# Kernel optimization log

Measured on AMD Instinct MI355X. Metric: run time of the kernel, lower is better.

Reference implementation:

```python
import jax, jax.numpy as jnp
import numpy as np

N = 50000      # nodes
E = 400000     # edges (avg degree 8)
G = 256        # graphs in batch
H = 256        # hidden_dim
DEPTH = 6
A, C, X, EF = 16, 8, 3, 16  # a_t, c_t, x_t, e_t feature dims (node_feats=27)


def setup_inputs() -> dict:
    key = jax.random.key(0)
    ks = jax.random.split(key, 16)
    s = lambda i, shape, sc=1.0: jax.random.normal(ks[i], shape, jnp.float32) * sc
    return {
        "a_t": s(0, (N, A)),
        "c_t": s(1, (N, C)),
        "x_t": s(2, (N, X)),
        "e_t": s(3, (E, EF)),
        "src": jax.random.randint(ks[4], (E,), 0, N),
        "dst": jax.random.randint(ks[5], (E,), 0, N),
        "graph_id": jnp.sort(jax.random.randint(ks[6], (N,), 0, G)),
        "W_in": s(7, (A + C + X, H), 0.1), "b_in": jnp.zeros((H,), jnp.float32),
        "W_e": s(8, (EF, H), 0.1), "b_e": jnp.zeros((H,), jnp.float32),
        "Wc1": s(9, (DEPTH, H, H), 0.05), "bc1": jnp.zeros((DEPTH, H), jnp.float32),
        "g1": jnp.ones((DEPTH, H), jnp.float32), "be1": jnp.zeros((DEPTH, H), jnp.float32),
        "Wc2": s(10, (DEPTH, H, H), 0.05), "bc2": jnp.zeros((DEPTH, H), jnp.float32),
        "g2": jnp.ones((DEPTH, H), jnp.float32), "be2": jnp.zeros((DEPTH, H), jnp.float32),
        "W_head": s(11, (H, 1), 0.1), "b_head": jnp.zeros((1,), jnp.float32),
    }


def _ln(x, g, b):
    mu = jnp.mean(x, -1, keepdims=True)
    v = jnp.mean((x - mu) ** 2, -1, keepdims=True)
    return (x - mu) * jax.lax.rsqrt(v + 1e-5) * g + b


def reference(a_t, c_t, x_t, e_t, src, dst, graph_id,
              W_in, b_in, W_e, b_e,
              Wc1, bc1, g1, be1, Wc2, bc2, g2, be2,
              W_head, b_head):
    n = a_t.shape[0]
    ones_e = jnp.ones((src.shape[0],), jnp.float32)
    deg_out = jax.ops.segment_sum(ones_e, src, num_segments=n)
    deg_in = jax.ops.segment_sum(ones_e, dst, num_segments=n)
    # DGL GraphConv norm='both': 0 for isolated nodes (pow(0,-0.5)=inf -> 0)
    norm_o = jnp.where(deg_out > 0, jax.lax.rsqrt(jnp.maximum(deg_out, 1.0)), 0.0)
    norm_i = jnp.where(deg_in > 0, jax.lax.rsqrt(jnp.maximum(deg_in, 1.0)), 0.0)

    def gconv(x, W, b):
        h = (x * norm_o[:, None]) @ W            # [N,H] transform + src norm
        m = jax.ops.segment_sum(h[src], dst, num_segments=n)  # SpMM gather/scatter
        return m * norm_i[:, None] + b

    h = gconv(jnp.concatenate([a_t, c_t, x_t], -1), W_in, b_in)
    e = e_t @ W_e + b_e                          # edge_linear
    # copy_e + mean over in-edges
    e_mean = jax.ops.segment_sum(e, dst, num_segments=n) / jnp.maximum(deg_in, 1.0)[:, None]
    h = h + e_mean

    def body(hc, p):
        W1, b1, ga, ba, W2, b2, gb, bb = p
        t = jax.nn.silu(_ln(gconv(hc, W1, b1), ga, ba))
        t = jax.nn.silu(_ln(gconv(t, W2, b2), gb, bb))
        return t + hc, None  # skip is Identity (in_dim == out_dim)

    h, _ = jax.lax.scan(body, h, (Wc1, bc1, g1, be1, Wc2, bc2, g2, be2))

    cnt = jax.ops.segment_sum(jnp.ones((n,), jnp.float32), graph_id, num_segments=G)
    pooled = jax.ops.segment_sum(h, graph_id, num_segments=G) / jnp.maximum(cnt, 1.0)[:, None]
    # property='dipole' -> Softplus, tau=1.0
    return jax.nn.softplus((pooled @ W_head + b_head) / 1.0)
```

## Files before the change

### kernel.cpp

```cpp
#include <hip/hip_runtime.h>
#include <hip/hip_bf16.h>

#define N_NODES 50000
#define N_EDGES 400000
#define N_GRAPH 256
#define HID 256
#define DEPTH 6

typedef float f32x4 __attribute__((ext_vector_type(4)));
typedef int   i32x4 __attribute__((ext_vector_type(4)));

__device__ __forceinline__ float bf2f(unsigned short u) {
  unsigned v = ((unsigned)u) << 16;
  return __builtin_bit_cast(float, v);
}
__device__ __forceinline__ unsigned short f2bf(float f) {
  unsigned u = __builtin_bit_cast(unsigned, f);
  u += 0x7fffu + ((u >> 16) & 1u);
  return (unsigned short)(u >> 16);
}

__device__ __forceinline__ float block_sum256(float v, float* lds) {
#pragma unroll
  for (int off = 32; off > 0; off >>= 1) v += __shfl_down(v, off, 64);
  int w = threadIdx.x >> 6;
  if ((threadIdx.x & 63) == 0) lds[w] = v;
  __syncthreads();
  float r = lds[0] + lds[1] + lds[2] + lds[3];
  __syncthreads();
  return r;
}

__global__ __launch_bounds__(256) void k_deg(const int* __restrict__ src, const int* __restrict__ dst,
                                             int* deg_out, int* deg_in) {
  int e = blockIdx.x * 256 + threadIdx.x;
  if (e < N_EDGES) { atomicAdd(&deg_out[src[e]], 1); atomicAdd(&deg_in[dst[e]], 1); }
}

__global__ __launch_bounds__(256) void k_norm(const int* deg_out, const int* deg_in,
                                              float* norm_o, float* norm_i) {
  int i = blockIdx.x * 256 + threadIdx.x;
  if (i < N_NODES) {
    int dO = deg_out[i], dI = deg_in[i];
    norm_o[i] = dO > 0 ? rsqrtf((float)dO) : 0.f;
    norm_i[i] = dI > 0 ? rsqrtf((float)dI) : 0.f;
  }
}

__global__ __launch_bounds__(256) void k_scan1(const int* deg_in, int* partial) {
  int i = blockIdx.x * 256 + threadIdx.x;
  int v = (i < N_NODES) ? deg_in[i] : 0;
#pragma unroll
  for (int off = 32; off > 0; off >>= 1) v += __shfl_down(v, off, 64);
  __shared__ int l[4];
  if ((threadIdx.x & 63) == 0) l[threadIdx.x >> 6] = v;
  __syncthreads();
  if (threadIdx.x == 0) partial[blockIdx.x] = l[0] + l[1] + l[2] + l[3];
}

__global__ __launch_bounds__(256) void k_scan2(const int* partial, int* chunk_off, int* row_start, int nb) {
  __shared__ int ss[256];
  int t = threadIdx.x;
  int v = (t < nb) ? partial[t] : 0;
  ss[t] = v; __syncthreads();
#pragma unroll
  for (int off = 1; off < 256; off <<= 1) {
    int x = ss[t];
    int y = (t >= off) ? ss[t - off] : 0;
    __syncthreads();
    ss[t] = x + y;
    __syncthreads();
  }
  if (t < nb) chunk_off[t] = ss[t] - v;
  if (t == 0) row_start[N_NODES] = N_EDGES;
}

__global__ __launch_bounds__(256) void k_scan3(const int* deg_in, const int* chunk_off, int* row_start) {
  __shared__ int ss[256];
  int t = threadIdx.x;
  int i = blockIdx.x * 256 + t;
  int v = (i < N_NODES) ? deg_in[i] : 0;
  ss[t] = v; __syncthreads();
#pragma unroll
  for (int off = 1; off < 256; off <<= 1) {
    int x = ss[t];
    int y = (t >= off) ? ss[t - off] : 0;
    __syncthreads();
    ss[t] = x + y;
    __syncthreads();
  }
  if (i < N_NODES) row_start[i] = chunk_off[blockIdx.x] + ss[t] - v;
}

__global__ __launch_bounds__(256) void k_fill(const int* src, const int* dst, const int* row_start,
                                              int* cursor, int* csr_src) {
  int e = blockIdx.x * 256 + threadIdx.x;
  if (e < N_EDGES) {
    int d = dst[e];
    int p = atomicAdd(&cursor[d], 1);
    csr_src[row_start[d] + p] = src[e];
  }
}

__global__ __launch_bounds__(256) void k_esum(const float* __restrict__ e_t, const int* __restrict__ dst,
                                              float* esum) {
  int t = blockIdx.x * 256 + threadIdx.x;
  int e = t >> 4, ch = t & 15;
  if (e < N_EDGES) atomicAdd(&esum[(size_t)dst[e] * 16 + ch], e_t[(size_t)e * 16 + ch]);
}

__global__ __launch_bounds__(256) void k_wt(const float* __restrict__ Wc1, const float* __restrict__ Wc2,
                                            unsigned short* __restrict__ Wt) {
  __shared__ float tile[32][33];
  int li = blockIdx.z;
  const float* W = ((li & 1) ? Wc2 : Wc1) + (size_t)(li >> 1) * HID * HID;
  int k0 = blockIdx.x * 32, n0 = blockIdx.y * 32;
  int tx = threadIdx.x & 31, ty = threadIdx.x >> 5;
#pragma unroll
  for (int r = ty; r < 32; r += 8) tile[r][tx] = W[(size_t)(k0 + r) * HID + n0 + tx];
  __syncthreads();
  unsigned short* outp = Wt + (size_t)li * HID * HID;
#pragma unroll
  for (int r = ty; r < 32; r += 8) outp[(size_t)(n0 + r) * HID + k0 + tx] = f2bf(tile[tx][r]);
}

__global__ __launch_bounds__(256) void k_z(const float* __restrict__ a, const float* __restrict__ c,
                                           const float* __restrict__ x, const float* __restrict__ norm_o,
                                           float* __restrict__ z) {
  int t = blockIdx.x * 256 + threadIdx.x;
  int n = t >> 5, lane = t & 31;
  if (n >= N_NODES) return;
  float v = 0.f;
  if (lane < 16) v = a[(size_t)n * 16 + lane];
  else if (lane < 24) v = c[(size_t)n * 8 + (lane - 16)];
  else if (lane < 27) v = x[(size_t)n * 3 + (lane - 24)];
  z[(size_t)n * 32 + lane] = v * norm_o[n];
}

__global__ __launch_bounds__(256) void k_in(const float* __restrict__ z, const float* __restrict__ esum,
                                            const int* __restrict__ csr_src, const int* __restrict__ rs,
                                            const float* __restrict__ norm_o, const float* __restrict__ norm_i,
                                            const float* __restrict__ W_in, const float* __restrict__ b_in,
                                            const float* __restrict__ W_e, const float* __restrict__ b_e,
                                            unsigned short* __restrict__ hf, unsigned short* __restrict__ Af) {
  int w = threadIdx.x >> 6, lane = threadIdx.x & 63;
  int n = blockIdx.x * 4 + w;
  int half = lane >> 5, ch = lane & 31;
  __shared__ float zs[4][32];
  __shared__ float es[4][16];
  if (lane >= 32 && lane < 48) es[w][lane - 32] = esum[(size_t)n * 16 + (lane - 32)];
  int beg = rs[n], end = rs[n + 1];
  float acc = 0.f;
  const float* zb = z + ch;
  int p = beg + half;
  for (; p + 6 < end; p += 8) {
    int s0 = csr_src[p], s1 = csr_src[p + 2], s2 = csr_src[p + 4], s3 = csr_src[p + 6];
    float v0 = zb[(size_t)s0 * 32], v1 = zb[(size_t)s1 * 32];
    float v2 = zb[(size_t)s2 * 32], v3 = zb[(size_t)s3 * 32];
    acc += (v0 + v1) + (v2 + v3);
  }
  for (; p < end; p += 2) acc += zb[(size_t)csr_src[p] * 32];
  acc += __shfl_xor(acc, 32, 64);
  if (lane < 32) zs[w][ch] = acc;
  __syncthreads();
  float degf = (float)(end - beg);
  float invd = 1.f / fmaxf(degf, 1.f);
  float niv = norm_i[n], nov = norm_o[n];
#pragma unroll
  for (int i = 0; i < 4; ++i) {
    int cc = lane + 64 * i;
    float da = 0.f, de = 0.f;
#pragma unroll
    for (int k = 0; k < 27; ++k) da += zs[w][k] * W_in[k * HID + cc];
#pragma unroll
    for (int k = 0; k < 16; ++k) de += es[w][k] * W_e[k * HID + cc];
    float val = da * niv + b_in[cc] + (de + degf * b_e[cc]) * invd;
    hf[(size_t)n * HID + cc] = f2bf(val);
    Af[(size_t)n * HID + cc] = f2bf(val * nov);
  }
}

template <int RES>
__global__ __launch_bounds__(512) void k_layer(const unsigned short* __restrict__ Af,
                                               const int* __restrict__ csr_src, const int* __restrict__ rs,
                                               const unsigned short* __restrict__ Bt,
                                               const float* __restrict__ norm_i,
                                               const float* __restrict__ norm_o,
                                               const float* __restrict__ b, const float* __restrict__ g,
                                               const float* __restrict__ be,
                                               unsigned short* __restrict__ hf,
                                               unsigned short* __restrict__ AfN) {
  const int LDA = HID + 8;
  __shared__ unsigned short As[16 * LDA];
  __shared__ float red1[8][16], red2[8][16];
  int wave = threadIdx.x >> 6, lane = threadIdx.x & 63;
  int l15 = lane & 15, quad = lane >> 4;
  int n0 = blockIdx.x * 16;
  int off = lane * 4;
  int r0 = wave * 2;
  int beg = rs[n0 + r0], mid = rs[n0 + r0 + 1], end = rs[n0 + r0 + 2];
  float lo0 = 0.f, lo1 = 0.f, lo2 = 0.f, lo3 = 0.f;
  float hi0 = 0.f, hi1 = 0.f, hi2 = 0.f, hi3 = 0.f;
  int p = beg;
  for (; p + 8 <= end; p += 8) {
    int s[8];
#pragma unroll
    for (int q = 0; q < 8; ++q) s[q] = csr_src[p + q];
    ushort4 rr[8];
#pragma unroll
    for (int q = 0; q < 8; ++q) rr[q] = *(const ushort4*)(Af + (size_t)s[q] * HID + off);
#pragma unroll
    for (int q = 0; q < 8; ++q) {
      float v0 = bf2f(rr[q].x), v1 = bf2f(rr[q].y), v2 = bf2f(rr[q].z), v3 = bf2f(rr[q].w);
      if (p + q >= mid) { hi0 += v0; hi1 += v1; hi2 += v2; hi3 += v3; }
      else             { lo0 += v0; lo1 += v1; lo2 += v2; lo3 += v3; }
    }
  }
  for (; p < end; ++p) {
    ushort4 r = *(const ushort4*)(Af + (size_t)csr_src[p] * HID + off);
    float v0 = bf2f(r.x), v1 = bf2f(r.y), v2 = bf2f(r.z), v3 = bf2f(r.w);
    if (p >= mid) { hi0 += v0; hi1 += v1; hi2 += v2; hi3 += v3; }
    else          { lo0 += v0; lo1 += v1; lo2 += v2; lo3 += v3; }
  }
  ushort4 o;
  o.x = f2bf(lo0); o.y = f2bf(lo1); o.z = f2bf(lo2); o.w = f2bf(lo3);
  *(ushort4*)(&As[(size_t)r0 * LDA + off]) = o;
  o.x = f2bf(hi0); o.y = f2bf(hi1); o.z = f2bf(hi2); o.w = f2bf(hi3);
  *(ushort4*)(&As[(size_t)(r0 + 1) * LDA + off]) = o;
  __syncthreads();
  const unsigned short* asp = &As[(size_t)l15 * LDA + quad * 8];
  const unsigned short* bp = Bt + (size_t)(wave * 32 + l15) * HID + quad * 8;
  f32x4 acc[2] = {};
  asm volatile("s_nop 7\n\ts_nop 7" : "+v"(acc[0]), "+v"(acc[1]));
#pragma unroll
  for (int k0 = 0; k0 < HID; k0 += 32) {
    i32x4 af = *(const i32x4*)(asp + k0);
#pragma unroll
    for (int t = 0; t < 2; ++t) {
      i32x4 bt = *(const i32x4*)(bp + (size_t)t * 16 * HID + k0);
      asm volatile("v_mfma_f32_16x16x32_bf16 %0, %1, %2, %0" : "+v"(acc[t]) : "v"(af), "v"(bt));
    }
  }
  asm volatile("s_nop 7\n\ts_nop 7\n\ts_nop 7" : "+v"(acc[0]), "+v"(acc[1]));
  float ni[4];
#pragma unroll
  for (int j = 0; j < 4; ++j) ni[j] = norm_i[n0 + quad * 4 + j];
#pragma unroll
  for (int t = 0; t < 2; ++t) {
    int ct = wave * 32 + t * 16 + l15;
    float bv = b[ct];
#pragma unroll
    for (int j = 0; j < 4; ++j) acc[t][j] = acc[t][j] * ni[j] + bv;
  }
  float s1[4] = {0.f, 0.f, 0.f, 0.f}, s2[4] = {0.f, 0.f, 0.f, 0.f};
#pragma unroll
  for (int t = 0; t < 2; ++t)
#pragma unroll
    for (int j = 0; j < 4; ++j) { s1[j] += acc[t][j]; s2[j] += acc[t][j] * acc[t][j]; }
#pragma unroll
  for (int m = 1; m < 16; m <<= 1) {
#pragma unroll
    for (int j = 0; j < 4; ++j) {
      s1[j] += __shfl_xor(s1[j], m, 16);
      s2[j] += __shfl_xor(s2[j], m, 16);
    }
  }
  if (l15 == 0) {
#pragma unroll
    for (int j = 0; j < 4; ++j) {
      red1[wave][quad * 4 + j] = s1[j];
      red2[wave][quad * 4 + j] = s2[j];
    }
  }
  __syncthreads();
  float mu[4], inv[4];
#pragma unroll
  for (int j = 0; j < 4; ++j) {
    int r = quad * 4 + j;
    float t1 = 0.f, t2 = 0.f;
#pragma unroll
    for (int ww = 0; ww < 8; ++ww) { t1 += red1[ww][r]; t2 += red2[ww][r]; }
    mu[j] = t1 * (1.f / HID);
    float var = t2 * (1.f / HID) - mu[j] * mu[j];
    inv[j] = rsqrtf(var + 1e-5f);
  }
#pragma unroll
  for (int j = 0; j < 4; ++j) {
    int r = n0 + quad * 4 + j;
    float nov = norm_o[r];
    unsigned short* hrow = hf + (size_t)r * HID;
    unsigned short* an = AfN + (size_t)r * HID;
#pragma unroll
    for (int t = 0; t < 2; ++t) {
      int ct = wave * 32 + t * 16 + l15;
      float oo = (acc[t][j] - mu[j]) * inv[j] * g[ct] + be[ct];
      float sl = oo * (1.f / (1.f + __expf(-oo)));
      float outv = sl;
      if (RES) {
        outv = sl + bf2f(hrow[ct]);
        hrow[ct] = f2bf(outv);
      }
      an[ct] = f2bf(outv * nov);
    }
  }
}

__global__ __launch_bounds__(256) void k_poolhead(const unsigned short* __restrict__ hf,
                                                  const int* __restrict__ gid,
                                                  const float* __restrict__ Wh, const float* __restrict__ bh,
                                                  float* __restrict__ out) {
  int gg = blockIdx.x, ch = threadIdx.x;
  int lo = 0, hi = N_NODES;
  while (lo < hi) { int mid = (lo + hi) >> 1; if (gid[mid] < gg) lo = mid + 1; else hi = mid; }
  int beg = lo;
  hi = N_NODES;
  while (lo < hi) { int mid = (lo + hi) >> 1; if (gid[mid] < gg + 1) lo = mid + 1; else hi = mid; }
  int end = lo;
  float s = 0.f;
  int n = beg;
  for (; n + 4 <= end; n += 4) {
    s += bf2f(hf[(size_t)n * HID + ch]) + bf2f(hf[(size_t)(n + 1) * HID + ch]) +
         bf2f(hf[(size_t)(n + 2) * HID + ch]) + bf2f(hf[(size_t)(n + 3) * HID + ch]);
  }
  for (; n < end; ++n) s += bf2f(hf[(size_t)n * HID + ch]);
  float v = s * Wh[ch];
  __shared__ float l[4];
  float tot = block_sum256(v, l);
  if (ch == 0) {
    float c = fmaxf((float)(end - beg), 1.f);
    float xx = tot / c + bh[0];
    out[gg] = fmaxf(xx, 0.f) + log1pf(expf(-fabsf(xx)));
  }
}

extern "C" void kernel_launch(void* const* d_in, const int* in_sizes, int n_in,
                              void* d_out, int out_size, void* d_ws, size_t ws_size,
                              hipStream_t stream) {
  const float* a_t = (const float*)d_in[0];
  const float* c_t = (const float*)d_in[1];
  const float* x_t = (const float*)d_in[2];
  const float* e_t = (const float*)d_in[3];
  const int* src = (const int*)d_in[4];
  const int* dst = (const int*)d_in[5];
  const int* gid = (const int*)d_in[6];
  const float* W_in = (const float*)d_in[7];
  const float* b_in = (const float*)d_in[8];
  const float* W_e  = (const float*)d_in[9];
  const float* b_e  = (const float*)d_in[10];
  const float* Wc1  = (const float*)d_in[11];
  const float* bc1  = (const float*)d_in[12];
  const float* g1   = (const float*)d_in[13];
  const float* be1  = (const float*)d_in[14];
  const float* Wc2  = (const float*)d_in[15];
  const float* bc2  = (const float*)d_in[16];
  const float* g2   = (const float*)d_in[17];
  const float* be2  = (const float*)d_in[18];
  const float* W_head = (const float*)d_in[19];
  const float* b_head = (const float*)d_in[20];
  float* out = (float*)d_out;

  char* base = (char*)d_ws;
  size_t off = 0;
  auto carve = [&](size_t bytes) -> void* {
    void* p = base + off;
    off += (bytes + 255) & ~(size_t)255;
    return p;
  };
  int*   deg_out = (int*)carve((size_t)N_NODES * 4);
  int*   deg_in  = (int*)carve((size_t)N_NODES * 4);
  int*   cursor  = (int*)carve((size_t)N_NODES * 4);
  float* esum    = (float*)carve((size_t)N_NODES * 16 * 4);
  size_t zbytes = off;
  float* norm_o  = (float*)carve((size_t)N_NODES * 4);
  float* norm_i  = (float*)carve((size_t)N_NODES * 4);
  int*   row_start = (int*)carve((size_t)(N_NODES + 1) * 4);
  int*   partial   = (int*)carve(256 * 4);
  int*   chunk_off = (int*)carve(256 * 4);
  int*   csr_src   = (int*)carve((size_t)N_EDGES * 4);
  unsigned short* Wt = (unsigned short*)carve((size_t)2 * DEPTH * HID * HID * 2);
  float* zpack = (float*)carve((size_t)N_NODES * 32 * 4);
  unsigned short* hf = (unsigned short*)carve((size_t)N_NODES * HID * 2);
  unsigned short* Af0 = (unsigned short*)carve((size_t)N_NODES * HID * 2);
  unsigned short* Af1 = (unsigned short*)carve((size_t)N_NODES * HID * 2);
  (void)ws_size; (void)in_sizes; (void)n_in; (void)out_size;

  hipMemsetAsync(d_ws, 0, zbytes, stream);

  int ebl = (N_EDGES + 255) / 256;
  int nbl = (N_NODES + 255) / 256;
  k_deg<<<ebl, 256, 0, stream>>>(src, dst, deg_out, deg_in);
  k_norm<<<nbl, 256, 0, stream>>>(deg_out, deg_in, norm_o, norm_i);
  k_scan1<<<nbl, 256, 0, stream>>>(deg_in, partial);
  k_scan2<<<1, 256, 0, stream>>>(partial, chunk_off, row_start, nbl);
  k_scan3<<<nbl, 256, 0, stream>>>(deg_in, chunk_off, row_start);
  k_fill<<<ebl, 256, 0, stream>>>(src, dst, row_start, cursor, csr_src);
  k_esum<<<(N_EDGES * 16 + 255) / 256, 256, 0, stream>>>(e_t, dst, esum);
  k_wt<<<dim3(8, 8, 2 * DEPTH), 256, 0, stream>>>(Wc1, Wc2, Wt);
  k_z<<<(N_NODES * 32 + 255) / 256, 256, 0, stream>>>(a_t, c_t, x_t, norm_o, zpack);
  k_in<<<N_NODES / 4, 256, 0, stream>>>(zpack, esum, csr_src, row_start,
                                        norm_o, norm_i, W_in, b_in, W_e, b_e, hf, Af0);
  int gbl = N_NODES / 16;
  for (int d = 0; d < DEPTH; ++d) {
    k_layer<0><<<gbl, 512, 0, stream>>>(Af0, csr_src, row_start, Wt + (size_t)(2 * d) * HID * HID,
                                        norm_i, norm_o, bc1 + d * HID, g1 + d * HID, be1 + d * HID, hf, Af1);
    k_layer<1><<<gbl, 512, 0, stream>>>(Af1, csr_src, row_start, Wt + (size_t)(2 * d + 1) * HID * HID,
                                        norm_i, norm_o, bc2 + d * HID, g2 + d * HID, be2 + d * HID, hf, Af0);
  }
  k_poolhead<<<N_GRAPH, 256, 0, stream>>>(hf, gid, W_head, b_head, out);
}
```

Before: 1.443 ms.

## Use one node per wave in layer gather with 16-byte loads

The fused gather+GEMM layer kernel now handles 8 nodes per block instead of 16. Each wave gathers one node's neighbours, with its two half-waves splitting the edges and each lane loading 16 bytes (8 bf16). The partial sums are combined with a cross-half shuffle, and the unused MFMA rows are zero-padded. The input-layer gather is likewise vectorised to float4 per lane with 8 edges in flight. This aims to cut the divergent lo/hi accumulation and raise memory-level parallelism per wave, at the cost of doubling the block count and wasting half of each 16-row MFMA tile.

```diff
diff --git a/kernel.cpp b/kernel.cpp
--- a/kernel.cpp
+++ b/kernel.cpp
@@ -18,6 +18,12 @@
   unsigned u = __builtin_bit_cast(unsigned, f);
   u += 0x7fffu + ((u >> 16) & 1u);
   return (unsigned short)(u >> 16);
+}
+__device__ __forceinline__ float bflo(unsigned u) {
+  return __builtin_bit_cast(float, u << 16);
+}
+__device__ __forceinline__ float bfhi(unsigned u) {
+  return __builtin_bit_cast(float, u & 0xffff0000u);
 }
 
 __device__ __forceinline__ float block_sum256(float v, float* lds) {
@@ -145,23 +151,25 @@
                                             unsigned short* __restrict__ hf, unsigned short* __restrict__ Af) {
   int w = threadIdx.x >> 6, lane = threadIdx.x & 63;
   int n = blockIdx.x * 4 + w;
-  int half = lane >> 5, ch = lane & 31;
+  int g = lane >> 3, c4 = lane & 7;
   __shared__ float zs[4][32];
   __shared__ float es[4][16];
   if (lane >= 32 && lane < 48) es[w][lane - 32] = esum[(size_t)n * 16 + (lane - 32)];
   int beg = rs[n], end = rs[n + 1];
-  float acc = 0.f;
-  const float* zb = z + ch;
-  int p = beg + half;
-  for (; p + 6 < end; p += 8) {
-    int s0 = csr_src[p], s1 = csr_src[p + 2], s2 = csr_src[p + 4], s3 = csr_src[p + 6];
-    float v0 = zb[(size_t)s0 * 32], v1 = zb[(size_t)s1 * 32];
-    float v2 = zb[(size_t)s2 * 32], v3 = zb[(size_t)s3 * 32];
-    acc += (v0 + v1) + (v2 + v3);
-  }
-  for (; p < end; p += 2) acc += zb[(size_t)csr_src[p] * 32];
-  acc += __shfl_xor(acc, 32, 64);
-  if (lane < 32) zs[w][ch] = acc;
+  f32x4 acc = {0.f, 0.f, 0.f, 0.f};
+  for (int p = beg + g; p < end; p += 8) {
+    int s = csr_src[p];
+    acc += *(const f32x4*)(z + (size_t)s * 32 + c4 * 4);
+  }
+#pragma unroll
+  for (int m = 8; m < 64; m <<= 1) {
+#pragma unroll
+    for (int k = 0; k < 4; ++k) acc[k] += __shfl_xor(acc[k], m, 64);
+  }
+  if (g == 0) {
+#pragma unroll
+    for (int k = 0; k < 4; ++k) zs[w][c4 * 4 + k] = acc[k];
+  }
   __syncthreads();
   float degf = (float)(end - beg);
   float invd = 1.f / fmaxf(degf, 1.f);
@@ -192,41 +200,55 @@
                                                unsigned short* __restrict__ AfN) {
   const int LDA = HID + 8;
   __shared__ unsigned short As[16 * LDA];
-  __shared__ float red1[8][16], red2[8][16];
+  __shared__ float red1[8][8], red2[8][8];
   int wave = threadIdx.x >> 6, lane = threadIdx.x & 63;
   int l15 = lane & 15, quad = lane >> 4;
-  int n0 = blockIdx.x * 16;
-  int off = lane * 4;
-  int r0 = wave * 2;
-  int beg = rs[n0 + r0], mid = rs[n0 + r0 + 1], end = rs[n0 + r0 + 2];
-  float lo0 = 0.f, lo1 = 0.f, lo2 = 0.f, lo3 = 0.f;
-  float hi0 = 0.f, hi1 = 0.f, hi2 = 0.f, hi3 = 0.f;
-  int p = beg;
-  for (; p + 8 <= end; p += 8) {
-    int s[8];
-#pragma unroll
-    for (int q = 0; q < 8; ++q) s[q] = csr_src[p + q];
-    ushort4 rr[8];
-#pragma unroll
-    for (int q = 0; q < 8; ++q) rr[q] = *(const ushort4*)(Af + (size_t)s[q] * HID + off);
-#pragma unroll
-    for (int q = 0; q < 8; ++q) {
-      float v0 = bf2f(rr[q].x), v1 = bf2f(rr[q].y), v2 = bf2f(rr[q].z), v3 = bf2f(rr[q].w);
-      if (p + q >= mid) { hi0 += v0; hi1 += v1; hi2 += v2; hi3 += v3; }
-      else             { lo0 += v0; lo1 += v1; lo2 += v2; lo3 += v3; }
+  int n0 = blockIdx.x * 8;
+  int half = lane >> 5, ch16 = lane & 31;
+  int boff = ch16 * 8;
+  {
+    ushort4 zz = {0, 0, 0, 0};
+    *(ushort4*)(&As[(size_t)(8 + wave) * LDA + lane * 4]) = zz;
+  }
+  int n = n0 + wave;
+  int beg = rs[n], end = rs[n + 1];
+  float a0 = 0.f, a1 = 0.f, a2 = 0.f, a3 = 0.f, a4 = 0.f, a5 = 0.f, a6 = 0.f, a7 = 0.f;
+  int p = beg + half;
+  for (; p + 6 < end; p += 8) {
+    int s0 = csr_src[p], s1 = csr_src[p + 2], s2 = csr_src[p + 4], s3 = csr_src[p + 6];
+    i32x4 v0 = *(const i32x4*)(Af + (size_t)s0 * HID + boff);
+    i32x4 v1 = *(const i32x4*)(Af + (size_t)s1 * HID + boff);
+    i32x4 v2 = *(const i32x4*)(Af + (size_t)s2 * HID + boff);
+    i32x4 v3 = *(const i32x4*)(Af + (size_t)s3 * HID + boff);
+#pragma unroll
+    for (int k = 0; k < 4; ++k) {
+      unsigned u0 = (unsigned)v0[k], u1 = (unsigned)v1[k], u2 = (unsigned)v2[k], u3 = (unsigned)v3[k];
+      float lo = bflo(u0) + bflo(u1) + bflo(u2) + bflo(u3);
+      float hi = bfhi(u0) + bfhi(u1) + bfhi(u2) + bfhi(u3);
+      if (k == 0) { a0 += lo; a1 += hi; }
+      else if (k == 1) { a2 += lo; a3 += hi; }
+      else if (k == 2) { a4 += lo; a5 += hi; }
+      else { a6 += lo; a7 += hi; }
     }
   }
-  for (; p < end; ++p) {
-    ushort4 r = *(const ushort4*)(Af + (size_t)csr_src[p] * HID + off);
-    float v0 = bf2f(r.x), v1 = bf2f(r.y), v2 = bf2f(r.z), v3 = bf2f(r.w);
-    if (p >= mid) { hi0 += v0; hi1 += v1; hi2 += v2; hi3 += v3; }
-    else          { lo0 += v0; lo1 += v1; lo2 += v2; lo3 += v3; }
-  }
-  ushort4 o;
-  o.x = f2bf(lo0); o.y = f2bf(lo1); o.z = f2bf(lo2); o.w = f2bf(lo3);
-  *(ushort4*)(&As[(size_t)r0 * LDA + off]) = o;
-  o.x = f2bf(hi0); o.y = f2bf(hi1); o.z = f2bf(hi2); o.w = f2bf(hi3);
-  *(ushort4*)(&As[(size_t)(r0 + 1) * LDA + off]) = o;
+  for (; p < end; p += 2) {
+    i32x4 v = *(const i32x4*)(Af + (size_t)csr_src[p] * HID + boff);
+    a0 += bflo(v[0]); a1 += bfhi(v[0]);
+    a2 += bflo(v[1]); a3 += bfhi(v[1]);
+    a4 += bflo(v[2]); a5 += bfhi(v[2]);
+    a6 += bflo(v[3]); a7 += bfhi(v[3]);
+  }
+  a0 += __shfl_xor(a0, 32, 64); a1 += __shfl_xor(a1, 32, 64);
+  a2 += __shfl_xor(a2, 32, 64); a3 += __shfl_xor(a3, 32, 64);
+  a4 += __shfl_xor(a4, 32, 64); a5 += __shfl_xor(a5, 32, 64);
+  a6 += __shfl_xor(a6, 32, 64); a7 += __shfl_xor(a7, 32, 64);
+  if (half == 0) {
+    ushort4 o0, o1;
+    o0.x = f2bf(a0); o0.y = f2bf(a1); o0.z = f2bf(a2); o0.w = f2bf(a3);
+    o1.x = f2bf(a4); o1.y = f2bf(a5); o1.z = f2bf(a6); o1.w = f2bf(a7);
+    *(ushort4*)(&As[(size_t)wave * LDA + boff]) = o0;
+    *(ushort4*)(&As[(size_t)wave * LDA + boff + 4]) = o1;
+  }
   __syncthreads();
   const unsigned short* asp = &As[(size_t)l15 * LDA + quad * 8];
   const unsigned short* bp = Bt + (size_t)(wave * 32 + l15) * HID + quad * 8;
@@ -244,7 +266,10 @@
   asm volatile("s_nop 7\n\ts_nop 7\n\ts_nop 7" : "+v"(acc[0]), "+v"(acc[1]));
   float ni[4];
 #pragma unroll
-  for (int j = 0; j < 4; ++j) ni[j] = norm_i[n0 + quad * 4 + j];
+  for (int j = 0; j < 4; ++j) {
+    int rl = quad * 4 + j;
+    ni[j] = norm_i[n0 + (rl & 7)];
+  }
 #pragma unroll
   for (int t = 0; t < 2; ++t) {
     int ct = wave * 32 + t * 16 + l15;
@@ -265,7 +290,7 @@
       s2[j] += __shfl_xor(s2[j], m, 16);
     }
   }
-  if (l15 == 0) {
+  if (l15 == 0 && quad < 2) {
 #pragma unroll
     for (int j = 0; j < 4; ++j) {
       red1[wave][quad * 4 + j] = s1[j];
@@ -276,31 +301,33 @@
   float mu[4], inv[4];
 #pragma unroll
   for (int j = 0; j < 4; ++j) {
-    int r = quad * 4 + j;
+    int rl = (quad * 4 + j) & 7;
     float t1 = 0.f, t2 = 0.f;
 #pragma unroll
-    for (int ww = 0; ww < 8; ++ww) { t1 += red1[ww][r]; t2 += red2[ww][r]; }
+    for (int ww = 0; ww < 8; ++ww) { t1 += red1[ww][rl]; t2 += red2[ww][rl]; }
     mu[j] = t1 * (1.f / HID);
     float var = t2 * (1.f / HID) - mu[j] * mu[j];
     inv[j] = rsqrtf(var + 1e-5f);
   }
-#pragma unroll
-  for (int j = 0; j < 4; ++j) {
-    int r = n0 + quad * 4 + j;
-    float nov = norm_o[r];
-    unsigned short* hrow = hf + (size_t)r * HID;
-    unsigned short* an = AfN + (size_t)r * HID;
-#pragma unroll
-    for (int t = 0; t < 2; ++t) {
-      int ct = wave * 32 + t * 16 + l15;
-      float oo = (acc[t][j] - mu[j]) * inv[j] * g[ct] + be[ct];
-      float sl = oo * (1.f / (1.f + __expf(-oo)));
-      float outv = sl;
-      if (RES) {
-        outv = sl + bf2f(hrow[ct]);
-        hrow[ct] = f2bf(outv);
+  if (quad < 2) {
+#pragma unroll
+    for (int j = 0; j < 4; ++j) {
+      int r = n0 + quad * 4 + j;
+      float nov = norm_o[r];
+      unsigned short* hrow = hf + (size_t)r * HID;
+      unsigned short* an = AfN + (size_t)r * HID;
+#pragma unroll
+      for (int t = 0; t < 2; ++t) {
+        int ct = wave * 32 + t * 16 + l15;
+        float oo = (acc[t][j] - mu[j]) * inv[j] * g[ct] + be[ct];
+        float sl = oo * (1.f / (1.f + __expf(-oo)));
+        float outv = sl;
+        if (RES) {
+          outv = sl + bf2f(hrow[ct]);
+          hrow[ct] = f2bf(outv);
+        }
+        an[ct] = f2bf(outv * nov);
       }
-      an[ct] = f2bf(outv * nov);
     }
   }
 }
@@ -399,7 +426,7 @@
   k_z<<<(N_NODES * 32 + 255) / 256, 256, 0, stream>>>(a_t, c_t, x_t, norm_o, zpack);
   k_in<<<N_NODES / 4, 256, 0, stream>>>(zpack, esum, csr_src, row_start,
                                         norm_o, norm_i, W_in, b_in, W_e, b_e, hf, Af0);
-  int gbl = N_NODES / 16;
+  int gbl = N_NODES / 8;
   for (int d = 0; d < DEPTH; ++d) {
     k_layer<0><<<gbl, 512, 0, stream>>>(Af0, csr_src, row_start, Wt + (size_t)(2 * d) * HID * HID,
                                         norm_i, norm_o, bc1 + d * HID, g1 + d * HID, be1 + d * HID, hf, Af1);
```

Result: slower. 1.845 ms (+27.9%).
